# Optimization experiments

Measured on AMD Instinct MI355X. Metric: run time of the kernel, lower is better.

## Reference

```python
import jax, jax.numpy as jnp
import numpy as np

DIM = 2048
K_DIM = 2048
HQ = 16          # query heads
HKV = 4          # kv heads
HD = DIM // HQ   # head dim = 128
KV_DIM = HD * HKV
MAX_LEN = 4096
THETA = 10000.0
ROPE_FACTOR = 8.0
CAUSAL = True
SCALE = HD ** -0.5


def rope_cos_sin(n):
    # mirrors generate_sin_cos_pos_emb (rope_factor > 1 branch)
    idx = jnp.arange(0, HD, 2, dtype=jnp.float32) / HD
    seq_len_eff = max(n, MAX_LEN)  # static python ints
    base_adjustment = (ROPE_FACTOR * seq_len_eff / MAX_LEN - (ROPE_FACTOR - 1.0)) ** (HD / (HD - 2))
    inv_freq = 1.0 / (THETA * base_adjustment) ** idx
    pos = jnp.arange(n, dtype=jnp.float32)
    if not CAUSAL:
        pos = pos - (n - 1) // 2
    freqs = pos[:, None] * inv_freq[None, :]          # [n, HD/2]
    emb = jnp.concatenate([freqs, freqs], axis=-1)    # [n, HD]
    return jnp.cos(emb), jnp.sin(emb)


def rotate_half(x):
    x1, x2 = jnp.split(x, 2, axis=-1)
    return jnp.concatenate([-x2, x1], axis=-1)


def setup_inputs() -> dict:
    key = jax.random.key(0)
    ks = jax.random.split(key, 11)
    B, N = 2, 2048
    s = 0.02
    return {
        "query": jax.random.normal(ks[0], (B, N, DIM), jnp.float32),
        "key": jax.random.normal(ks[1], (B, N, K_DIM), jnp.float32),
        "value": jax.random.normal(ks[2], (B, N, K_DIM), jnp.float32),
        "Wq": jax.random.normal(ks[3], (DIM, DIM), jnp.float32) * s,
        "bq": jnp.zeros((DIM,), jnp.float32),
        "Wk": jax.random.normal(ks[4], (KV_DIM, K_DIM), jnp.float32) * s,
        "bk": jnp.zeros((KV_DIM,), jnp.float32),
        "Wv": jax.random.normal(ks[5], (KV_DIM, K_DIM), jnp.float32) * s,
        "bv": jnp.zeros((KV_DIM,), jnp.float32),
        "Wo": jax.random.normal(ks[6], (DIM, DIM), jnp.float32) * s,
        "bo": jnp.zeros((DIM,), jnp.float32),
    }


def reference(query, key, value, Wq, bq, Wk, bk, Wv, bv, Wo, bo):
    b, n, _ = query.shape
    q = query @ Wq.T + bq                       # [b, n, DIM]
    k = key @ Wk.T + bk                         # [b, n, KV_DIM]
    v = value @ Wv.T + bv                       # [b, n, KV_DIM]
    q = q.reshape(b, n, HQ, HD).transpose(0, 2, 1, 3)    # [b, HQ, n, d]
    k = k.reshape(b, n, HKV, HD).transpose(0, 2, 1, 3)   # [b, HKV, n, d]
    v = v.reshape(b, n, HKV, HD).transpose(0, 2, 1, 3)
    cos, sin = rope_cos_sin(n)                  # [n, HD] each, broadcast over b,h
    q = q * cos + rotate_half(q) * sin
    k = k * cos + rotate_half(k) * sin
    g = HQ // HKV
    qg = q.reshape(b, HKV, g, n, HD)            # group query heads per kv head
    scores = jnp.einsum('bhgnd,bhsd->bhgns', qg * SCALE, k)  # [b, HKV, g, n, s]
    if CAUSAL:
        causal = jnp.tril(jnp.ones((n, n), dtype=bool))
        scores = jnp.where(causal[None, None, None], scores, jnp.finfo(scores.dtype).min)
    attn = jax.nn.softmax(scores, axis=-1)
    out = jnp.einsum('bhgns,bhsd->bhgnd', attn, v)           # [b, HKV, g, n, d]
    out = out.reshape(b, HQ, n, HD).transpose(0, 2, 1, 3).reshape(b, n, DIM)
    return out @ Wo.T + bo
```

## Files before the change

### kernel.cpp

```cpp
#include <hip/hip_runtime.h>
#include <cstdint>


typedef __bf16 bf16_t;
typedef __attribute__((ext_vector_type(8))) __bf16 bf16x8;
typedef __attribute__((ext_vector_type(4))) float f32x4;

#define B_    2
#define N_    2048
#define DIM_  2048
#define HQ_   16
#define HKV_  4
#define HD_   128
#define KVD_  512
#define SCALE_ 0.08838834764831845f

static __device__ __forceinline__ void ld_g2l(void* lds, const void* g) {
  __builtin_amdgcn_global_load_lds((__attribute__((address_space(1))) void*)g,
                                   (__attribute__((address_space(3))) void*)lds,
                                   16, 0, 0);
}

static __device__ __forceinline__ f32x4 vmax4(f32x4 a, f32x4 b) {
  f32x4 r;
  r[0] = fmaxf(a[0], b[0]); r[1] = fmaxf(a[1], b[1]);
  r[2] = fmaxf(a[2], b[2]); r[3] = fmaxf(a[3], b[3]);
  return r;
}

__global__ void k_sincos(float* __restrict__ cosT, float* __restrict__ sinT) {
  int idx = blockIdx.x * 256 + threadIdx.x;
  int i = idx & 63;
  int n = idx >> 6;
  float inv = expf(-(float)i * (9.210340371976184f / 64.0f));
  float ang = (float)n * inv;
  cosT[idx] = cosf(ang);
  sinT[idx] = sinf(ang);
}

__global__ void k_cvt3(const float* __restrict__ s0, bf16_t* __restrict__ d0, int n0,
                       const float* __restrict__ s1, bf16_t* __restrict__ d1, int n1,
                       const float* __restrict__ s2, bf16_t* __restrict__ d2, int n2)
{
  int i = (blockIdx.x * 256 + threadIdx.x) * 4;
  const float* s; bf16_t* d; int off;
  if (i < n0)                { s = s0; d = d0; off = i; }
  else if (i < n0 + n1)      { s = s1; d = d1; off = i - n0; }
  else if (i < n0 + n1 + n2) { s = s2; d = d2; off = i - n0 - n1; }
  else return;
  f32x4 v = *(const f32x4*)(s + off);
  union { bf16_t h[4]; uint2 u; } pk;
  pk.h[0] = (bf16_t)v[0]; pk.h[1] = (bf16_t)v[1];
  pk.h[2] = (bf16_t)v[2]; pk.h[3] = (bf16_t)v[3];
  *(uint2*)(d + off) = pk.u;
}

template <int AMODE, bool CF32>
static __device__ __forceinline__ void gemm_body(
    const void* __restrict__ Av, const bf16_t* __restrict__ W,
    const float* __restrict__ bias, void* __restrict__ Cv,
    int N, int K, int bm, int bn, bf16_t* As, bf16_t* Bs)
{
  const int tid  = threadIdx.x;
  const int lane = tid & 63;
  const int wave = tid >> 6;
  const int l15  = lane & 15;
  const int lg   = lane >> 4;
  const int wr = (wave >> 1) * 64, wc = (wave & 1) * 64;

  f32x4 acc[4][4] = {};

  uint8_t* AsB = (uint8_t*)As;
  uint8_t* BsB = (uint8_t*)Bs;
  const uint8_t* Wbase = (const uint8_t*)W + (size_t)(bn * 128) * K * 2;
  const uint8_t* AbaseB = (const uint8_t*)Av + (size_t)(bm * 128) * K * 2;

  for (int k0 = 0; k0 < K; k0 += 64) {
    for (int r = 0; r < 4; ++r) {
      int o = r * 4096 + wave * 1024 + lane * 16;
      int row = o >> 7;
      int colB = (o & 127) ^ ((row & 7) << 4);
      ld_g2l(BsB + r * 4096 + wave * 1024,
             Wbase + (size_t)row * (K * 2) + (size_t)k0 * 2 + colB);
    }
    if (AMODE == 1) {
      for (int r = 0; r < 4; ++r) {
        int o = r * 4096 + wave * 1024 + lane * 16;
        int row = o >> 7;
        int colB = (o & 127) ^ ((row & 7) << 4);
        ld_g2l(AsB + r * 4096 + wave * 1024,
               AbaseB + (size_t)row * (K * 2) + (size_t)k0 * 2 + colB);
      }
    } else {
      for (int i = 0; i < 4; ++i) {
        int c = i * 256 + tid;
        int row = c >> 3;
        int k8  = (c & 7) * 8;
        const float* ap = (const float*)Av + (size_t)(bm * 128 + row) * K + k0 + k8;
        f32x4 alo = *(const f32x4*)ap;
        f32x4 ahi = *(const f32x4*)(ap + 4);
        bf16x8 va;
        va[0] = (bf16_t)alo[0]; va[1] = (bf16_t)alo[1];
        va[2] = (bf16_t)alo[2]; va[3] = (bf16_t)alo[3];
        va[4] = (bf16_t)ahi[0]; va[5] = (bf16_t)ahi[1];
        va[6] = (bf16_t)ahi[2]; va[7] = (bf16_t)ahi[3];
        int sw = (k8 * 2) ^ ((row & 7) << 4);
        *(bf16x8*)(AsB + row * 128 + sw) = va;
      }
    }
    __syncthreads();
    for (int kk = 0; kk < 2; ++kk) {
      const int koff = kk * 64 + (lg << 4);
      bf16x8 fa[4], fb[4];
      for (int fi = 0; fi < 4; ++fi) {
        int row = wr + fi * 16 + l15;
        fa[fi] = *(const bf16x8*)(AsB + row * 128 + (koff ^ ((row & 7) << 4)));
      }
      for (int fj = 0; fj < 4; ++fj) {
        int row = wc + fj * 16 + l15;
        fb[fj] = *(const bf16x8*)(BsB + row * 128 + (koff ^ ((row & 7) << 4)));
      }
      for (int fi = 0; fi < 4; ++fi)
        for (int fj = 0; fj < 4; ++fj)
          acc[fi][fj] = __builtin_amdgcn_mfma_f32_16x16x32_bf16(
              fa[fi], fb[fj], acc[fi][fj], 0, 0, 0);
    }
    __syncthreads();
  }

  const int r0 = lg * 4;
  for (int fi = 0; fi < 4; ++fi) {
    for (int rr = 0; rr < 4; ++rr) {
      int grow = bm * 128 + wr + fi * 16 + r0 + rr;
      size_t rowoff = (size_t)grow * N;
      for (int fj = 0; fj < 4; ++fj) {
        int gcol = bn * 128 + wc + fj * 16 + l15;
        float v = acc[fi][fj][rr] + bias[gcol];
        if (CF32) ((float*)Cv)[rowoff + gcol] = v;
        else      ((bf16_t*)Cv)[rowoff + gcol] = (bf16_t)v;
      }
    }
  }
}

__global__ __launch_bounds__(256, 4) void k_gemm_qkv(
    const float* __restrict__ q, const bf16_t* __restrict__ Wqb,
    const float* __restrict__ bq, bf16_t* __restrict__ Qp,
    const float* __restrict__ k, const bf16_t* __restrict__ Wkb,
    const float* __restrict__ bk, bf16_t* __restrict__ Kp,
    const float* __restrict__ v, const bf16_t* __restrict__ Wvb,
    const float* __restrict__ bv, bf16_t* __restrict__ Vp)
{
  __shared__ bf16_t As[128 * 64];
  __shared__ bf16_t Bs[128 * 64];
  const int z = blockIdx.z;
  if (z != 0 && blockIdx.y >= 4) return;
  const float* A; const bf16_t* W; const float* bias; bf16_t* C; int Nn;
  if (z == 0)      { A = q; W = Wqb; bias = bq; C = Qp; Nn = 2048; }
  else if (z == 1) { A = k; W = Wkb; bias = bk; C = Kp; Nn = 512; }
  else             { A = v; W = Wvb; bias = bv; C = Vp; Nn = 512; }
  gemm_body<0, false>(A, W, bias, C, Nn, 2048, blockIdx.x, blockIdx.y, As, Bs);
}

__global__ __launch_bounds__(256, 4) void k_gemm_o(
    const bf16_t* __restrict__ Ain, const bf16_t* __restrict__ Wob,
    const float* __restrict__ bo, float* __restrict__ out)
{
  __shared__ bf16_t As[128 * 64];
  __shared__ bf16_t Bs[128 * 64];
  gemm_body<1, true>(Ain, Wob, bo, out, 2048, 2048, blockIdx.x, blockIdx.y, As, Bs);
}

__global__ void k_rope(bf16_t* __restrict__ X, const float* __restrict__ cosT,
                       const float* __restrict__ sinT, int lgnh, float outScale)
{
  int idx = blockIdx.x * 256 + threadIdx.x;
  int j = idx & 7;
  int h = (idx >> 3) & ((1 << lgnh) - 1);
  int row = idx >> (3 + lgnh);
  int n = row & (N_ - 1);
  int d0 = j * 8;
  const float* cp = cosT + (n << 6) + d0;
  const float* sp = sinT + (n << 6) + d0;
  f32x4 c0 = *(const f32x4*)cp,  c1 = *(const f32x4*)(cp + 4);
  f32x4 s0 = *(const f32x4*)sp,  s1 = *(const f32x4*)(sp + 4);
  bf16_t* xb = X + (size_t)row * (size_t)(128 << lgnh) + (h << 7) + d0;
  bf16x8 x1 = *(const bf16x8*)xb;
  bf16x8 x2 = *(const bf16x8*)(xb + 64);
  bf16x8 o1, o2;
#pragma unroll
  for (int e = 0; e < 8; ++e) {
    float c = e < 4 ? c0[e] : c1[e - 4];
    float s = e < 4 ? s0[e] : s1[e - 4];
    float a = (float)x1[e], bvl = (float)x2[e];
    o1[e] = (bf16_t)((a * c - bvl * s) * outScale);
    o2[e] = (bf16_t)((bvl * c + a * s) * outScale);
  }
  *(bf16x8*)xb = o1;
  *(bf16x8*)(xb + 64) = o2;
}

__global__ void k_transpose_v(const bf16_t* __restrict__ Vp, bf16_t* __restrict__ Vt)
{
  __shared__ bf16_t tile[64][72];
  const int tid = threadIdx.x;
  const int r0 = blockIdx.x * 64;
  const int d0 = blockIdx.y * 64;
  for (int r = 0; r < 2; ++r) {
    int n = r * 32 + (tid >> 3);
    int dc = (tid & 7) * 8;
    *(uint4*)&tile[n][dc] = *(const uint4*)(Vp + (size_t)(r0 + n) * KVD_ + d0 + dc);
  }
  __syncthreads();
  const int b = r0 >> 11;
  const int nseq = r0 & (N_ - 1);
  for (int r = 0; r < 2; ++r) {
    int dd = r * 32 + (tid >> 3);
    int nc = (tid & 7) * 8;
    int dglob = d0 + dd;
    int hkv = dglob >> 7, dloc = dglob & 127;
    union { bf16_t h[8]; uint4 v; } pk;
    for (int j = 0; j < 8; ++j) pk.h[j] = tile[nc + j][dd];
    size_t drow = (size_t)(b * HKV_ + hkv) * 128 + dloc;
    *(uint4*)(Vt + drow * N_ + nseq + nc) = pk.v;
  }
}

__global__ __launch_bounds__(256, 2) void k_attn(
    const bf16_t* __restrict__ Qp, const bf16_t* __restrict__ Kp,
    const bf16_t* __restrict__ Vt, bf16_t* __restrict__ AO)
{
  __shared__ bf16_t Ks[2][64 * 128];
  __shared__ bf16_t Vs[2][128 * 64];
  __shared__ bf16_t Ps[4][16 * 72];
  const int tid = threadIdx.x, lane = tid & 63, wave = tid >> 6;
  const int l15 = lane & 15, lg = lane >> 4;
  const int bx = 15 - (int)blockIdx.x;
  const int qtile = bx * 4 + wave;
  const int bh = blockIdx.y;
  const int b = bh >> 4, hq = bh & 15, hkv = hq >> 2;

  bf16x8 qf[2][4];
  for (int rf = 0; rf < 2; ++rf) {
    size_t qrow = (size_t)b * N_ + qtile * 32 + rf * 16 + l15;
    const uint8_t* qb = (const uint8_t*)Qp + (qrow * DIM_ + (size_t)hq * HD_) * 2 + lg * 16;
    for (int ks = 0; ks < 4; ++ks)
      qf[rf][ks] = *(const bf16x8*)(qb + ks * 64);
  }

  float m[2] = {-1e30f, -1e30f};
  float ln[2] = {0.f, 0.f};
  f32x4 o[2][8] = {};

  const uint8_t* KpB = (const uint8_t*)Kp + ((size_t)b * N_ * KVD_ + (size_t)hkv * HD_) * 2;
  const uint8_t* VtB = (const uint8_t*)Vt + (size_t)(b * HKV_ + hkv) * HD_ * (size_t)N_ * 2;
  uint8_t* PwB = (uint8_t*)Ps[wave];

  const int Tw   = qtile / 2 + 1;
  const int Tmax = 2 * bx + 2;

  auto stage = [&](int buf, int t) {
    uint8_t* KsB = (uint8_t*)Ks[buf];
    uint8_t* VsB = (uint8_t*)Vs[buf];
#pragma unroll
    for (int r = 0; r < 4; ++r) {
      int o16 = r * 4096 + wave * 1024 + lane * 16;
      int row = o16 >> 8;
      int colB = (o16 & 255) ^ ((row & 7) << 4);
      ld_g2l(KsB + r * 4096 + wave * 1024,
             KpB + (size_t)(t * 64 + row) * (KVD_ * 2) + colB);
    }
#pragma unroll
    for (int r = 0; r < 4; ++r) {
      int o16 = r * 4096 + wave * 1024 + lane * 16;
      int dd = o16 >> 7;
      int colB = (o16 & 127) ^ ((dd & 7) << 4);
      ld_g2l(VsB + r * 4096 + wave * 1024,
             VtB + (size_t)dd * (N_ * 2) + t * 128 + colB);
    }
  };

  stage(0, 0);
  __syncthreads();
  int cur = 0;

  for (int t = 0; t < Tmax; ++t) {
    if (t + 1 < Tmax) stage(cur ^ 1, t + 1);

    if (t < Tw) {
      const uint8_t* KsB = (const uint8_t*)Ks[cur];
      const uint8_t* VsB = (const uint8_t*)Vs[cur];

      f32x4 s4[2][4] = {};
      __builtin_amdgcn_s_setprio(1);
#pragma unroll
      for (int ks = 0; ks < 4; ++ks) {
        int koff = ks * 64 + lg * 16;
#pragma unroll
        for (int kb = 0; kb < 4; ++kb) {
          int row = kb * 16 + l15;
          bf16x8 kf = *(const bf16x8*)(KsB + row * 256 + (koff ^ ((row & 7) << 4)));
          s4[0][kb] = __builtin_amdgcn_mfma_f32_16x16x32_bf16(kf, qf[0][ks], s4[0][kb], 0, 0, 0);
          s4[1][kb] = __builtin_amdgcn_mfma_f32_16x16x32_bf16(kf, qf[1][ks], s4[1][kb], 0, 0, 0);
        }
      }
      __builtin_amdgcn_s_setprio(0);

      if (t == Tw - 1) {
#pragma unroll
        for (int rf = 0; rf < 2; ++rf) {
          int q = qtile * 32 + rf * 16 + l15;
#pragma unroll
          for (int kb = 0; kb < 4; ++kb) {
            int key = t * 64 + kb * 16 + lg * 4;
#pragma unroll
            for (int rr = 0; rr < 4; ++rr)
              if (key + rr > q) s4[rf][kb][rr] = -1e30f;
          }
        }
      }

      bf16x8 pf[2][2];
#pragma unroll
      for (int rf = 0; rf < 2; ++rf) {
        f32x4 mx = vmax4(vmax4(s4[rf][0], s4[rf][1]), vmax4(s4[rf][2], s4[rf][3]));
        float rm = fmaxf(fmaxf(mx[0], mx[1]), fmaxf(mx[2], mx[3]));
        rm = fmaxf(rm, __shfl_xor(rm, 16));
        rm = fmaxf(rm, __shfl_xor(rm, 32));
        float mn = fmaxf(m[rf], rm);
        float sc = __expf(m[rf] - mn);

        f32x4 p[4];
        f32x4 psum = {0.f, 0.f, 0.f, 0.f};
#pragma unroll
        for (int kb = 0; kb < 4; ++kb) {
#pragma unroll
          for (int rr = 0; rr < 4; ++rr)
            p[kb][rr] = __expf(s4[rf][kb][rr] - mn);
          psum += p[kb];
        }
        float rs = (psum[0] + psum[1]) + (psum[2] + psum[3]);
        rs += __shfl_xor(rs, 16);
        rs += __shfl_xor(rs, 32);
        ln[rf] = ln[rf] * sc + rs;
        m[rf] = mn;

#pragma unroll
        for (int db = 0; db < 8; ++db) o[rf][db] *= sc;

#pragma unroll
        for (int kb = 0; kb < 4; ++kb) {
          union { bf16_t h[4]; uint2 u; } pk;
          pk.h[0] = (bf16_t)p[kb][0]; pk.h[1] = (bf16_t)p[kb][1];
          pk.h[2] = (bf16_t)p[kb][2]; pk.h[3] = (bf16_t)p[kb][3];
          *(uint2*)(PwB + l15 * 144 + kb * 32 + lg * 8) = pk.u;
        }
        pf[rf][0] = *(const bf16x8*)(PwB + l15 * 144 + lg * 16);
        pf[rf][1] = *(const bf16x8*)(PwB + l15 * 144 + 64 + lg * 16);
      }

      __builtin_amdgcn_s_setprio(1);
#pragma unroll
      for (int ks2 = 0; ks2 < 2; ++ks2) {
        int koff = ks2 * 64 + lg * 16;
#pragma unroll
        for (int db = 0; db < 8; ++db) {
          int dd = db * 16 + l15;
          bf16x8 vf = *(const bf16x8*)(VsB + dd * 128 + (koff ^ ((dd & 7) << 4)));
          o[0][db] = __builtin_amdgcn_mfma_f32_16x16x32_bf16(vf, pf[0][ks2], o[0][db], 0, 0, 0);
          o[1][db] = __builtin_amdgcn_mfma_f32_16x16x32_bf16(vf, pf[1][ks2], o[1][db], 0, 0, 0);
        }
      }
      __builtin_amdgcn_s_setprio(0);
    }

    __syncthreads();
    cur ^= 1;
  }

#pragma unroll
  for (int rf = 0; rf < 2; ++rf) {
    float iv = 1.f / ln[rf];
    size_t qrow = (size_t)b * N_ + qtile * 32 + rf * 16 + l15;
    uint8_t* ob = (uint8_t*)(AO + qrow * DIM_ + (size_t)hq * HD_);
#pragma unroll
    for (int db = 0; db < 8; ++db) {
      union { bf16_t h[4]; uint2 u; } pk;
      pk.h[0] = (bf16_t)(o[rf][db][0] * iv);
      pk.h[1] = (bf16_t)(o[rf][db][1] * iv);
      pk.h[2] = (bf16_t)(o[rf][db][2] * iv);
      pk.h[3] = (bf16_t)(o[rf][db][3] * iv);
      *(uint2*)(ob + (db * 16 + lg * 4) * 2) = pk.u;
    }
  }
}

extern "C" void kernel_launch(void* const* d_in, const int* in_sizes, int n_in,
                              void* d_out, int out_size, void* d_ws, size_t ws_size,
                              hipStream_t stream)
{
  if (ws_size < (46u << 20)) return;

  const float* query = (const float*)d_in[0];
  const float* key   = (const float*)d_in[1];
  const float* value = (const float*)d_in[2];
  const float* Wq = (const float*)d_in[3];
  const float* bq = (const float*)d_in[4];
  const float* Wk = (const float*)d_in[5];
  const float* bk = (const float*)d_in[6];
  const float* Wv = (const float*)d_in[7];
  const float* bv = (const float*)d_in[8];
  const float* Wo = (const float*)d_in[9];
  const float* bo = (const float*)d_in[10];
  float* out = (float*)d_out;

  uint8_t* ws = (uint8_t*)d_ws;
  float*  cosT = (float*)(ws);
  float*  sinT = (float*)(ws + (512u << 10));
  bf16_t* Qp   = (bf16_t*)(ws + (1u  << 20));
  bf16_t* Kp   = (bf16_t*)(ws + (17u << 20));
  bf16_t* Vp   = (bf16_t*)(ws + (21u << 20));
  bf16_t* Vt   = (bf16_t*)(ws + (25u << 20));
  bf16_t* Wqb  = (bf16_t*)(ws + (29u << 20));
  bf16_t* Wkb  = (bf16_t*)(ws + (37u << 20));
  bf16_t* Wvb  = (bf16_t*)(ws + (39u << 20));
  bf16_t* Wob  = (bf16_t*)(ws + (17u << 20));

  k_sincos<<<512, 256, 0, stream>>>(cosT, sinT);

  k_cvt3<<<6144, 256, 0, stream>>>(Wq, Wqb, 4194304,
                                   Wk, Wkb, 1048576,
                                   Wv, Wvb, 1048576);

  k_gemm_qkv<<<dim3(32, 16, 3), 256, 0, stream>>>(
      query, Wqb, bq, Qp, key, Wkb, bk, Kp, value, Wvb, bv, Vp);

  k_rope<<<2048, 256, 0, stream>>>(Qp, cosT, sinT, 4, SCALE_);
  k_rope<<<512,  256, 0, stream>>>(Kp, cosT, sinT, 2, 1.0f);

  k_transpose_v<<<dim3(64, 8), 256, 0, stream>>>(Vp, Vt);

  k_attn<<<dim3(16, 32), 256, 0, stream>>>(Qp, Kp, Vt, Qp);

  k_cvt3<<<4096, 256, 0, stream>>>(Wo, Wob, 4194304,
                                   nullptr, nullptr, 0,
                                   nullptr, nullptr, 0);

  k_gemm_o<<<dim3(32, 16), 256, 0, stream>>>(Qp, Wob, bo, out);
}
```

Before: 235.3 us.

## Double-buffer GEMM LDS tiles to overlap global loads with MFMA compute

Restructures the shared GEMM body to use two LDS buffers per operand. The next K-tile is prefetched (global-to-LDS for weights, fp32 A into registers) while MFMAs run on the current tile, with one barrier per iteration instead of two. Compute is bracketed with s_setprio, and launch bounds drop from 4 to 2 blocks per CU to make room for the doubled LDS and the extra registers. This trades occupancy for latency hiding in the QKV and output projections.

```diff
diff --git a/kernel.cpp b/kernel.cpp
--- a/kernel.cpp
+++ b/kernel.cpp
@@ -59,7 +59,8 @@
 static __device__ __forceinline__ void gemm_body(
     const void* __restrict__ Av, const bf16_t* __restrict__ W,
     const float* __restrict__ bias, void* __restrict__ Cv,
-    int N, int K, int bm, int bn, bf16_t* As, bf16_t* Bs)
+    int N, int K, int bm, int bn,
+    bf16_t* As0, bf16_t* As1, bf16_t* Bs0, bf16_t* Bs1)
 {
   const int tid  = threadIdx.x;
   const int lane = tid & 63;
@@ -70,69 +71,116 @@
 
   f32x4 acc[4][4] = {};
 
-  uint8_t* AsB = (uint8_t*)As;
-  uint8_t* BsB = (uint8_t*)Bs;
+  uint8_t* AsB[2] = {(uint8_t*)As0, (uint8_t*)As1};
+  uint8_t* BsB[2] = {(uint8_t*)Bs0, (uint8_t*)Bs1};
   const uint8_t* Wbase = (const uint8_t*)W + (size_t)(bn * 128) * K * 2;
   const uint8_t* AbaseB = (const uint8_t*)Av + (size_t)(bm * 128) * K * 2;
-
-  for (int k0 = 0; k0 < K; k0 += 64) {
+  const float*   Af = (const float*)Av;
+
+  f32x4 areg[8];
+
+  auto stageW = [&](int buf, int k0) {
+#pragma unroll
     for (int r = 0; r < 4; ++r) {
       int o = r * 4096 + wave * 1024 + lane * 16;
       int row = o >> 7;
       int colB = (o & 127) ^ ((row & 7) << 4);
-      ld_g2l(BsB + r * 4096 + wave * 1024,
+      ld_g2l(BsB[buf] + r * 4096 + wave * 1024,
              Wbase + (size_t)row * (K * 2) + (size_t)k0 * 2 + colB);
     }
-    if (AMODE == 1) {
-      for (int r = 0; r < 4; ++r) {
-        int o = r * 4096 + wave * 1024 + lane * 16;
-        int row = o >> 7;
-        int colB = (o & 127) ^ ((row & 7) << 4);
-        ld_g2l(AsB + r * 4096 + wave * 1024,
-               AbaseB + (size_t)row * (K * 2) + (size_t)k0 * 2 + colB);
-      }
-    } else {
-      for (int i = 0; i < 4; ++i) {
-        int c = i * 256 + tid;
-        int row = c >> 3;
-        int k8  = (c & 7) * 8;
-        const float* ap = (const float*)Av + (size_t)(bm * 128 + row) * K + k0 + k8;
-        f32x4 alo = *(const f32x4*)ap;
-        f32x4 ahi = *(const f32x4*)(ap + 4);
-        bf16x8 va;
-        va[0] = (bf16_t)alo[0]; va[1] = (bf16_t)alo[1];
-        va[2] = (bf16_t)alo[2]; va[3] = (bf16_t)alo[3];
-        va[4] = (bf16_t)ahi[0]; va[5] = (bf16_t)ahi[1];
-        va[6] = (bf16_t)ahi[2]; va[7] = (bf16_t)ahi[3];
-        int sw = (k8 * 2) ^ ((row & 7) << 4);
-        *(bf16x8*)(AsB + row * 128 + sw) = va;
-      }
-    }
-    __syncthreads();
+  };
+  auto stageA_g2l = [&](int buf, int k0) {
+#pragma unroll
+    for (int r = 0; r < 4; ++r) {
+      int o = r * 4096 + wave * 1024 + lane * 16;
+      int row = o >> 7;
+      int colB = (o & 127) ^ ((row & 7) << 4);
+      ld_g2l(AsB[buf] + r * 4096 + wave * 1024,
+             AbaseB + (size_t)row * (K * 2) + (size_t)k0 * 2 + colB);
+    }
+  };
+  auto loadA = [&](int k0) {
+#pragma unroll
+    for (int i = 0; i < 4; ++i) {
+      int c = i * 256 + tid;
+      int row = c >> 3;
+      int k8  = (c & 7) * 8;
+      const float* ap = Af + (size_t)(bm * 128 + row) * K + k0 + k8;
+      areg[i * 2]     = *(const f32x4*)ap;
+      areg[i * 2 + 1] = *(const f32x4*)(ap + 4);
+    }
+  };
+  auto writeA = [&](int buf) {
+#pragma unroll
+    for (int i = 0; i < 4; ++i) {
+      int c = i * 256 + tid;
+      int row = c >> 3;
+      int k8  = (c & 7) * 8;
+      bf16x8 va;
+      f32x4 lo = areg[i * 2], hi = areg[i * 2 + 1];
+      va[0] = (bf16_t)lo[0]; va[1] = (bf16_t)lo[1];
+      va[2] = (bf16_t)lo[2]; va[3] = (bf16_t)lo[3];
+      va[4] = (bf16_t)hi[0]; va[5] = (bf16_t)hi[1];
+      va[6] = (bf16_t)hi[2]; va[7] = (bf16_t)hi[3];
+      int sw = (k8 * 2) ^ ((row & 7) << 4);
+      *(bf16x8*)(AsB[buf] + row * 128 + sw) = va;
+    }
+  };
+  auto compute = [&](int buf) {
+    const uint8_t* A = AsB[buf];
+    const uint8_t* Bt = BsB[buf];
+    __builtin_amdgcn_s_setprio(1);
+#pragma unroll
     for (int kk = 0; kk < 2; ++kk) {
       const int koff = kk * 64 + (lg << 4);
       bf16x8 fa[4], fb[4];
+#pragma unroll
       for (int fi = 0; fi < 4; ++fi) {
         int row = wr + fi * 16 + l15;
-        fa[fi] = *(const bf16x8*)(AsB + row * 128 + (koff ^ ((row & 7) << 4)));
-      }
+        fa[fi] = *(const bf16x8*)(A + row * 128 + (koff ^ ((row & 7) << 4)));
+      }
+#pragma unroll
       for (int fj = 0; fj < 4; ++fj) {
         int row = wc + fj * 16 + l15;
-        fb[fj] = *(const bf16x8*)(BsB + row * 128 + (koff ^ ((row & 7) << 4)));
-      }
+        fb[fj] = *(const bf16x8*)(Bt + row * 128 + (koff ^ ((row & 7) << 4)));
+      }
+#pragma unroll
       for (int fi = 0; fi < 4; ++fi)
+#pragma unroll
         for (int fj = 0; fj < 4; ++fj)
           acc[fi][fj] = __builtin_amdgcn_mfma_f32_16x16x32_bf16(
               fa[fi], fb[fj], acc[fi][fj], 0, 0, 0);
     }
+    __builtin_amdgcn_s_setprio(0);
+  };
+
+  stageW(0, 0);
+  if (AMODE == 0) { loadA(0); writeA(0); }
+  else            { stageA_g2l(0, 0); }
+  __syncthreads();
+
+  int cur = 0;
+  for (int k0 = 0; k0 < K; k0 += 64) {
+    const bool pf = (k0 + 64 < K);
+    if (pf) {
+      stageW(cur ^ 1, k0 + 64);
+      if (AMODE == 0) loadA(k0 + 64);
+      else            stageA_g2l(cur ^ 1, k0 + 64);
+    }
+    compute(cur);
+    if (pf && AMODE == 0) writeA(cur ^ 1);
     __syncthreads();
+    cur ^= 1;
   }
 
   const int r0 = lg * 4;
+#pragma unroll
   for (int fi = 0; fi < 4; ++fi) {
+#pragma unroll
     for (int rr = 0; rr < 4; ++rr) {
       int grow = bm * 128 + wr + fi * 16 + r0 + rr;
       size_t rowoff = (size_t)grow * N;
+#pragma unroll
       for (int fj = 0; fj < 4; ++fj) {
         int gcol = bn * 128 + wc + fj * 16 + l15;
         float v = acc[fi][fj][rr] + bias[gcol];
@@ -143,7 +191,7 @@
   }
 }
 
-__global__ __launch_bounds__(256, 4) void k_gemm_qkv(
+__global__ __launch_bounds__(256, 2) void k_gemm_qkv(
     const float* __restrict__ q, const bf16_t* __restrict__ Wqb,
     const float* __restrict__ bq, bf16_t* __restrict__ Qp,
     const float* __restrict__ k, const bf16_t* __restrict__ Wkb,
@@ -151,24 +199,26 @@
     const float* __restrict__ v, const bf16_t* __restrict__ Wvb,
     const float* __restrict__ bv, bf16_t* __restrict__ Vp)
 {
-  __shared__ bf16_t As[128 * 64];
-  __shared__ bf16_t Bs[128 * 64];
+  __shared__ bf16_t As0[128 * 64], As1[128 * 64];
+  __shared__ bf16_t Bs0[128 * 64], Bs1[128 * 64];
   const int z = blockIdx.z;
   if (z != 0 && blockIdx.y >= 4) return;
   const float* A; const bf16_t* W; const float* bias; bf16_t* C; int Nn;
   if (z == 0)      { A = q; W = Wqb; bias = bq; C = Qp; Nn = 2048; }
   else if (z == 1) { A = k; W = Wkb; bias = bk; C = Kp; Nn = 512; }
   else             { A = v; W = Wvb; bias = bv; C = Vp; Nn = 512; }
-  gemm_body<0, false>(A, W, bias, C, Nn, 2048, blockIdx.x, blockIdx.y, As, Bs);
-}
-
-__global__ __launch_bounds__(256, 4) void k_gemm_o(
+  gemm_body<0, false>(A, W, bias, C, Nn, 2048, blockIdx.x, blockIdx.y,
+                      As0, As1, Bs0, Bs1);
+}
+
+__global__ __launch_bounds__(256, 2) void k_gemm_o(
     const bf16_t* __restrict__ Ain, const bf16_t* __restrict__ Wob,
     const float* __restrict__ bo, float* __restrict__ out)
 {
-  __shared__ bf16_t As[128 * 64];
-  __shared__ bf16_t Bs[128 * 64];
-  gemm_body<1, true>(Ain, Wob, bo, out, 2048, 2048, blockIdx.x, blockIdx.y, As, Bs);
+  __shared__ bf16_t As0[128 * 64], As1[128 * 64];
+  __shared__ bf16_t Bs0[128 * 64], Bs1[128 * 64];
+  gemm_body<1, true>(Ain, Wob, bo, out, 2048, 2048, blockIdx.x, blockIdx.y,
+                     As0, As1, Bs0, Bs1);
 }
 
 __global__ void k_rope(bf16_t* __restrict__ X, const float* __restrict__ cosT,
```

Result: slower. 283.7 us (+20.6%).
